# Kernel optimization log

Measured on AMD Instinct MI355X. Metric: run time of the kernel, lower is better.

The kernel has to match this reference:

```python
import jax, jax.numpy as jnp
import numpy as np

N_FLUID, N_BOX, K_MAX, KS, NCELL = 6000, 3000, 80, 4, 64
RADIUS = np.float32(0.5 * 1.5 * 6 * 0.025)  # filter_extent / 2 = 0.1125


def _ball_to_cube(p):
    """Volume-preserving ball->cube mapping (open3d ContinuousConv convention).
    p: [..., 3] coordinates in the unit ball; returns coords in [-1,1]^3."""
    eps = 1e-12
    x, y, z = p[..., 0], p[..., 1], p[..., 2]
    sq = x * x + y * y + z * z
    norm = jnp.sqrt(sq)
    rxy2 = x * x + y * y
    # sphere -> cylinder (volume preserving)
    polar = 1.25 * z * z > rxy2
    s_pol = jnp.sqrt(3.0 * norm / (norm + jnp.abs(z) + eps))
    s_eq = norm / jnp.sqrt(rxy2 + eps)
    xc = jnp.where(polar, s_pol * x, s_eq * x)
    yc = jnp.where(polar, s_pol * y, s_eq * y)
    zc = jnp.where(polar, jnp.sign(z) * norm, 1.5 * z * s_eq)
    zero = sq < 1e-12
    xc = jnp.where(zero, 0.0, xc)
    yc = jnp.where(zero, 0.0, yc)
    zc = jnp.where(zero, 0.0, zc)
    # cylinder -> cube (area-preserving disc -> square on xy)
    rxy = jnp.sqrt(xc * xc + yc * yc)
    FP = 4.0 / np.pi
    safe_x = jnp.where(jnp.abs(xc) < eps, eps, xc)
    safe_y = jnp.where(jnp.abs(yc) < eps, eps, yc)
    cond = jnp.abs(xc) >= jnp.abs(yc)
    u1 = jnp.sign(xc) * rxy
    v1 = u1 * FP * jnp.arctan(yc / safe_x)
    v2 = jnp.sign(yc) * rxy
    u2 = v2 * FP * jnp.arctan(xc / safe_y)
    u = jnp.where(cond, u1, u2)
    v = jnp.where(cond, v1, v2)
    small = rxy < eps
    u = jnp.where(small, 0.0, u)
    v = jnp.where(small, 0.0, v)
    return jnp.stack([u, v, zc], axis=-1)


def build_neighbors(pos_in, pos_out, ignore_self):
    """Fixed-radius neighbor search (capped at K_MAX) + window + trilinear
    interpolation cells/weights. Returns idx [No,K], cells [No,K,8] int32,
    coef [No,K,8] (trilinear weight * poly6 window * validity)."""
    d = pos_in[None, :, :] - pos_out[:, None, :]            # [No,Ni,3]
    d2 = jnp.sum(d * d, axis=-1)
    if ignore_self:
        ii = jnp.arange(pos_out.shape[0])
        d2 = jnp.where(ii[:, None] == ii[None, :], jnp.inf, d2)
    neg = jnp.where(d2 <= RADIUS * RADIUS, -d2, -jnp.inf)
    vals, idx = jax.lax.top_k(neg, K_MAX)                   # [No,K]
    valid = (vals > -jnp.inf).astype(pos_in.dtype)
    rel = (pos_in[idx] - pos_out[:, None, :]) / RADIUS      # [No,K,3] unit ball
    r2 = jnp.sum(rel * rel, axis=-1)
    win = jnp.clip((1.0 - r2) ** 3, 0.0, 1.0) * valid       # poly6 window
    g = jnp.clip((_ball_to_cube(rel) + 1.0) * 0.5 * (KS - 1), 0.0, KS - 1.0)
    i0 = jnp.clip(jnp.floor(g), 0, KS - 2).astype(jnp.int32)
    t = g - i0.astype(g.dtype)
    cells, tw = [], []
    for dx in (0, 1):
        for dy in (0, 1):
            for dz in (0, 1):
                w = ((t[..., 0] if dx else 1.0 - t[..., 0])
                     * (t[..., 1] if dy else 1.0 - t[..., 1])
                     * (t[..., 2] if dz else 1.0 - t[..., 2]))
                cell = ((i0[..., 2] + dz) * KS + (i0[..., 1] + dy)) * KS + (i0[..., 0] + dx)
                cells.append(cell)
                tw.append(w)
    cells = jnp.stack(cells, axis=-1)                       # [No,K,8]
    coef = jnp.stack(tw, axis=-1) * win[..., None]          # [No,K,8]
    return idx, cells, coef


def apply_cconv(feats_in, idx, cells, coef, W, b):
    """Continuous conv: scatter neighbor feats into 64 kernel cells per query,
    then contract with the filter. W: [64, F, O]."""
    N, K = idx.shape
    F = feats_in.shape[-1]
    nf = feats_in[idx]                                      # [N,K,F]
    S = jnp.zeros((N * NCELL, F), feats_in.dtype)
    row = (jnp.arange(N, dtype=jnp.int32) * NCELL)[:, None]
    for c in range(8):                                      # 8 trilinear corners
        flat = (row + cells[..., c]).reshape(-1)
        S = S.at[flat].add((coef[..., c:c + 1] * nf).reshape(-1, F))
    return jnp.einsum('ncf,cfo->no', S.reshape(N, NCELL, F), W) + b


def setup_inputs() -> dict:
    key = jax.random.key(0)
    ks = jax.random.split(key, 16)

    def p(i, shape, scale=0.05):
        return (scale * jax.random.normal(ks[i], shape)).astype(jnp.float32)

    return {
        'pos': jax.random.uniform(ks[0], (N_FLUID, 3), dtype=jnp.float32),
        'vel': jax.random.normal(ks[1], (N_FLUID, 3), dtype=jnp.float32),
        'box': jax.random.uniform(ks[2], (N_BOX, 3), dtype=jnp.float32),
        'box_feats': jax.random.normal(ks[3], (N_BOX, 3), dtype=jnp.float32),
        'cf_w': p(4, (NCELL, 4, 32)), 'cf_b': jnp.zeros((32,), jnp.float32),
        'co_w': p(5, (NCELL, 3, 32)), 'co_b': jnp.zeros((32,), jnp.float32),
        'd0_w': p(6, (4, 32)), 'd0_b': jnp.zeros((32,), jnp.float32),
        'c1_w': p(7, (NCELL, 96, 64)), 'c1_b': jnp.zeros((64,), jnp.float32),
        'd1_w': p(8, (96, 64)), 'd1_b': jnp.zeros((64,), jnp.float32),
        'c2_w': p(9, (NCELL, 64, 64)), 'c2_b': jnp.zeros((64,), jnp.float32),
        'd2_w': p(10, (64, 64)), 'd2_b': jnp.zeros((64,), jnp.float32),
        'c3_w': p(11, (NCELL, 64, 3)), 'c3_b': jnp.zeros((3,), jnp.float32),
        'd3_w': p(12, (64, 3)), 'd3_b': jnp.zeros((3,), jnp.float32),
    }


def reference(pos, vel, box, box_feats, cf_w, cf_b, co_w, co_b, d0_w, d0_b,
              c1_w, c1_b, d1_w, d1_b, c2_w, c2_b, d2_w, d2_b, c3_w, c3_b,
              d3_w, d3_b):
    fidx, fcells, fcoef = build_neighbors(pos, pos, True)
    oidx, ocells, ocoef = build_neighbors(box, pos, False)
    ff = jnp.concatenate([jnp.ones_like(pos[:, :1]), vel], axis=-1)  # [N,4]
    a_cf = apply_cconv(ff, fidx, fcells, fcoef, cf_w, cf_b)
    a_co = apply_cconv(box_feats, oidx, ocells, ocoef, co_w, co_b)
    a_d0 = ff @ d0_w + d0_b
    x = jnp.concatenate([a_co, a_cf, a_d0], axis=-1)                 # [N,96]
    for cw, cb, dw, db in ((c1_w, c1_b, d1_w, d1_b),
                           (c2_w, c2_b, d2_w, d2_b),
                           (c3_w, c3_b, d3_w, d3_b)):
        h = jax.nn.relu(x)
        y = apply_cconv(h, fidx, fcells, fcoef, cw, cb) + (h @ dw + db)
        x = y + x if y.shape[-1] == x.shape[-1] else y
    return x * (1.0 / 128.0)  # pos_correction [N,3]
```

## Files before the change

### kernel.cpp

```cpp
#include <hip/hip_runtime.h>
#include <math.h>

namespace {

constexpr int NQ  = 6000;
constexpr int NB  = 3000;
constexpr int K   = 80;
constexpr float RAD = 0.1125f;
constexpr float RADI = 1.0f / 0.1125f;
constexpr float R2  = RAD * RAD;
constexpr float EPSF = 1e-12f;

constexpr int GS  = 8;
constexpr int NC  = GS*GS*GS;
constexpr int NO  = 65 * 64;
constexpr int NBLK = (NQ + 3) / 4;
constexpr int NBLK8 = ((NBLK + 7) / 8) * 8;
constexpr int PREPB = 512;

typedef __attribute__((ext_vector_type(8))) short bf16x8;
typedef __attribute__((ext_vector_type(4))) float f32x4;

__device__ __forceinline__ float sgn(float x) {
    return (x > 0.f) ? 1.f : ((x < 0.f) ? -1.f : 0.f);
}

__device__ __forceinline__ unsigned int bf16rne(float f) {
    unsigned int u = __float_as_uint(f);
    return (u + 0x7fffu + ((u >> 16) & 1u)) >> 16;
}
__device__ __forceinline__ float bf16f(unsigned short u) {
    return __uint_as_float(((unsigned int)u) << 16);
}
__device__ __forceinline__ int cell_of(float x, float y, float z) {
    int cx = min(max((int)(x * (float)GS), 0), GS-1);
    int cy = min(max((int)(y * (float)GS), 0), GS-1);
    int cz = min(max((int)(z * (float)GS), 0), GS-1);
    return (cz*GS + cy)*GS + cx;
}

__device__ __forceinline__ void coef_compute(
    float ddx, float ddy, float ddz, int slot,
    int* __restrict__ cells, float* __restrict__ coefs)
{
    float rx = ddx * RADI, ry = ddy * RADI, rz = ddz * RADI;
    float r2 = rx*rx + ry*ry + rz*rz;
    float w1 = 1.f - r2;
    float win = (w1 > 0.f) ? w1*w1*w1 : 0.f;
    float norm = sqrtf(r2);
    float rxy2 = rx*rx + ry*ry;
    float xc, yc, zc;
    if (r2 < 1e-12f) {
        xc = yc = zc = 0.f;
    } else if (1.25f * rz * rz > rxy2) {
        float s = sqrtf(3.0f * norm / (norm + fabsf(rz) + EPSF));
        xc = s * rx; yc = s * ry; zc = sgn(rz) * norm;
    } else {
        float s = norm / sqrtf(rxy2 + EPSF);
        xc = s * rx; yc = s * ry; zc = 1.5f * rz * s;
    }
    float rxy = sqrtf(xc*xc + yc*yc);
    const float FP = (float)(4.0 / M_PI);
    float u, v;
    if (rxy < EPSF) {
        u = 0.f; v = 0.f;
    } else if (fabsf(xc) >= fabsf(yc)) {
        float sx = (fabsf(xc) < EPSF) ? EPSF : xc;
        u = sgn(xc) * rxy;
        v = u * FP * atanf(yc / sx);
    } else {
        float sy = (fabsf(yc) < EPSF) ? EPSF : yc;
        v = sgn(yc) * rxy;
        u = v * FP * atanf(xc / sy);
    }
    float gx = fminf(fmaxf((u  + 1.f) * 0.5f * 3.f, 0.f), 3.f);
    float gy = fminf(fmaxf((v  + 1.f) * 0.5f * 3.f, 0.f), 3.f);
    float gz = fminf(fmaxf((zc + 1.f) * 0.5f * 3.f, 0.f), 3.f);
    int ix = min((int)floorf(gx), 2);
    int iy = min((int)floorf(gy), 2);
    int iz = min((int)floorf(gz), 2);
    float tx = gx - (float)ix, ty = gy - (float)iy, tz = gz - (float)iz;
    cells[slot] = iz*16 + iy*4 + ix;
    float wx0 = 1.f - tx, wy0 = 1.f - ty, wz0 = 1.f - tz;
    float4 lo, hi;
    lo.x = wx0 * wy0 * wz0 * win;
    lo.y = wx0 * wy0 * tz  * win;
    lo.z = wx0 * ty  * wz0 * win;
    lo.w = wx0 * ty  * tz  * win;
    hi.x = tx  * wy0 * wz0 * win;
    hi.y = tx  * wy0 * tz  * win;
    hi.z = tx  * ty  * wz0 * win;
    hi.w = tx  * ty  * tz  * win;
    float4* cf = (float4*)(coefs + (size_t)slot * 8);
    cf[0] = lo; cf[1] = hi;
}

__global__ __launch_bounds__(1024) void grid_build_kernel(
    const float* __restrict__ pos, const float* __restrict__ box,
    int* __restrict__ gs_f, int* __restrict__ gs_b,
    int* __restrict__ cur_f, int* __restrict__ cur_b)
{
    __shared__ int cntF[NC], cntB[NC];
    __shared__ int tmpF[NC], tmpB[NC];
    int tid = threadIdx.x;
    int half = tid >> 9, t = tid & 511;
    if (half == 0) cntF[t] = 0; else cntB[t] = 0;
    __syncthreads();
    for (int i = tid; i < NQ + NB; i += 1024) {
        if (i < NQ) {
            atomicAdd(&cntF[cell_of(pos[i*3], pos[i*3+1], pos[i*3+2])], 1);
        } else {
            int b = i - NQ;
            atomicAdd(&cntB[cell_of(box[b*3], box[b*3+1], box[b*3+2])], 1);
        }
    }
    __syncthreads();
    int* cnt = half ? cntB : cntF;
    int* tmp = half ? tmpB : tmpF;
    int cv = cnt[t];
    tmp[t] = cv;
    __syncthreads();
    for (int off = 1; off < NC; off <<= 1) {
        int v = (t >= off) ? tmp[t - off] : 0;
        __syncthreads();
        tmp[t] += v;
        __syncthreads();
    }
    int* gsd = half ? gs_b : gs_f;
    int* cur = half ? cur_b : cur_f;
    int excl = tmp[t] - cv;
    gsd[t] = excl;
    cur[t] = excl;
    if (t == NC - 1) gsd[NC] = tmp[t];
}

__global__ __launch_bounds__(256) void scatter_pts_kernel(
    const float* __restrict__ pos, const float* __restrict__ box,
    int* __restrict__ cur_f, int* __restrict__ cur_b,
    float* __restrict__ spf, int* __restrict__ sif,
    float* __restrict__ spb, int* __restrict__ sib)
{
    int t = blockIdx.x * blockDim.x + threadIdx.x;
    if (t < NQ) {
        float x = pos[t*3], y = pos[t*3+1], z = pos[t*3+2];
        int dst = atomicAdd(&cur_f[cell_of(x,y,z)], 1);
        *reinterpret_cast<float4*>(spf + (size_t)dst*4) = make_float4(x, y, z, 0.f);
        sif[dst] = t;
    } else if (t < NQ + NB) {
        int b = t - NQ;
        float x = box[b*3], y = box[b*3+1], z = box[b*3+2];
        int dst = atomicAdd(&cur_b[cell_of(x,y,z)], 1);
        *reinterpret_cast<float4*>(spb + (size_t)dst*4) = make_float4(x, y, z, 0.f);
        sib[dst] = b;
    }
}

__global__ __launch_bounds__(256) void nn2gc_kernel(
    const float* __restrict__ pos,
    const float* __restrict__ spf, const int* __restrict__ sif, const int* __restrict__ gsf,
    const float* __restrict__ spb, const int* __restrict__ sib, const int* __restrict__ gsb,
    int* __restrict__ f_cnt, int* __restrict__ f_idx, float* __restrict__ f_d2,
    int* __restrict__ f_cell, float* __restrict__ f_coef,
    int* __restrict__ b_cnt, int* __restrict__ b_idx, float* __restrict__ b_d2,
    int* __restrict__ b_cell, float* __restrict__ b_coef,
    const float* __restrict__ c1w, const float* __restrict__ d1w,
    const float* __restrict__ c2w, const float* __restrict__ d2w,
    const float* __restrict__ c3w, const float* __restrict__ d3w,
    const float* __restrict__ vel, const float* __restrict__ bfeat,
    const float* __restrict__ cfw, const float* __restrict__ cow,
    const float* __restrict__ d0w, const float* __restrict__ d0b,
    unsigned short* __restrict__ Bt1, unsigned short* __restrict__ Bt2,
    unsigned short* __restrict__ G0f, unsigned short* __restrict__ G0b,
    float* __restrict__ W3p, float* __restrict__ x1)
{
    if (blockIdx.x < PREPB) {
        int stride = PREPB * 256;
        int gid = blockIdx.x * 256 + threadIdx.x;
        for (int i = gid; i < NQ * 1024; i += stride) {
            int j = i >> 10, rr = i & 1023, c = rr >> 4, op = (rr & 15) * 2;
            float vx = vel[j*3+0], vy = vel[j*3+1], vz = vel[j*3+2];
            const float* w = cfw + (size_t)c * 128;
            float s0 = w[op]   + vx*w[32+op]   + vy*w[64+op]   + vz*w[96+op];
            float s1 = w[op+1] + vx*w[32+op+1] + vy*w[64+op+1] + vz*w[96+op+1];
            *reinterpret_cast<unsigned int*>(G0f + (size_t)j * 2048 + c*32 + op) =
                bf16rne(s0) | (bf16rne(s1) << 16);
        }
        for (int i = gid; i < NB * 1024; i += stride) {
            int j = i >> 10, rr = i & 1023, c = rr >> 4, op = (rr & 15) * 2;
            float b0 = bfeat[j*3+0], b1 = bfeat[j*3+1], b2 = bfeat[j*3+2];
            const float* w = cow + (size_t)c * 96;
            float s0 = b0*w[op]   + b1*w[32+op]   + b2*w[64+op];
            float s1 = b0*w[op+1] + b1*w[32+op+1] + b2*w[64+op+1];
            *reinterpret_cast<unsigned int*>(G0b + (size_t)j * 2048 + c*32 + op) =
                bf16rne(s0) | (bf16rne(s1) << 16);
        }
        for (int i = gid; i < NO * 96; i += stride) {
            int n = i / 96, f = i % 96, c = n >> 6, o = n & 63;
            float v = (c < 64) ? c1w[((size_t)c*96 + f)*64 + o] : d1w[f*64 + o];
            Bt1[i] = (unsigned short)bf16rne(v);
        }
        for (int i = gid; i < NO * 64; i += stride) {
            int n = i / 64, f = i % 64, c = n >> 6, o = n & 63;
            float v = (c < 64) ? c2w[((size_t)c*64 + f)*64 + o] : d2w[f*64 + o];
            Bt2[i] = (unsigned short)bf16rne(v);
        }
        for (int i = gid; i < 64 * 195; i += stride) {
            int f = i / 195, r = i % 195, c = r / 3, o = r % 3;
            W3p[i] = (c < 64) ? c3w[(c*64 + f)*3 + o] : d3w[f*3 + o];
        }
        for (int i = gid; i < NQ * 32; i += stride) {
            int n = i >> 5, o = i & 31;
            float acc = d0b[o] + d0w[o]
                      + vel[n*3+0] * d0w[32 + o]
                      + vel[n*3+1] * d0w[64 + o]
                      + vel[n*3+2] * d0w[96 + o];
            x1[n*96 + 64 + o] = acc;
        }
        return;
    }
    int gw = (int)(blockIdx.x - PREPB) * 4 + ((int)threadIdx.x >> 6);
    int lane = threadIdx.x & 63;
    if (gw >= 2 * NQ) return;
    bool isF = gw < NQ;
    int wid = isF ? gw : gw - NQ;
    const float* sp = isF ? spf : spb;
    const int*   si = isF ? sif : sib;
    const int*   gs = isF ? gsf : gsb;
    int*   cnt   = isF ? f_cnt  : b_cnt;
    int*   idxs  = isF ? f_idx  : b_idx;
    float* d2s   = isF ? f_d2   : b_d2;
    int*   cells = isF ? f_cell : b_cell;
    float* coefs = isF ? f_coef : b_coef;
    int    tot   = isF ? NQ : NB;
    float qx = pos[wid*3+0], qy = pos[wid*3+1], qz = pos[wid*3+2];
    int cx = min(max((int)(qx * (float)GS), 0), GS-1);
    int cy = min(max((int)(qy * (float)GS), 0), GS-1);
    int cz = min(max((int)(qz * (float)GS), 0), GS-1);
    int x0 = max(cx-1, 0), x1c = min(cx+1, GS-1);
    int base = wid * K;
    int c = 0;

    auto process = [&](bool hit, int oj, float ddx, float ddy, float ddz, float d2) {
        unsigned long long m = __ballot(hit);
        int pc = __popcll(m);
        if (pc == 0) return;
        if (c + pc <= K) {
            if (hit) {
                int p = c + __popcll(m & ((1ull << lane) - 1ull));
                idxs[base + p] = oj;
                d2s [base + p] = d2;
                float* cf = coefs + (size_t)(base + p) * 8;
                cf[0] = ddx; cf[1] = ddy; cf[2] = ddz;
            }
            c += pc;
        } else {
            while (m) {
                int l = __ffsll((unsigned long long)m) - 1;
                m &= m - 1ull;
                float dd = __shfl(d2, l);
                int jv = __shfl(oj, l);
                float ax = __shfl(ddx, l), ay = __shfl(ddy, l), az = __shfl(ddz, l);
                int slot = -1;
                if (c < K) { slot = c; c++; }
                else {
                    float mx = -1.f; int am = 0;
                    for (int s = 0; s < K; ++s) {
                        float v = d2s[base + s];
                        if (v > mx) { mx = v; am = s; }
                    }
                    if (dd < mx) slot = am;
                }
                if (slot >= 0 && lane == 0) {
                    idxs[base + slot] = jv;
                    d2s [base + slot] = dd;
                    float* cf = coefs + (size_t)(base + slot) * 8;
                    cf[0] = ax; cf[1] = ay; cf[2] = az;
                }
            }
        }
    };

    int s0v[9], s1v[9];
#pragma unroll
    for (int r = 0; r < 9; ++r) {
        int z = cz + (r / 3) - 1, y = cy + (r % 3) - 1;
        bool ok = ((unsigned)z < (unsigned)GS) && ((unsigned)y < (unsigned)GS);
        int row = ok ? (z*GS + y)*GS : 0;
        int a0 = gs[row + x0];
        int a1 = gs[row + x1c + 1];
        s0v[r] = a0;
        s1v[r] = ok ? a1 : a0;
    }
    int    ojv[9];
    float4 pv [9];
#pragma unroll
    for (int r = 0; r < 9; ++r) {
        int a = min(s0v[r] + lane, tot - 1);
        ojv[r] = si[a];
        pv [r] = *reinterpret_cast<const float4*>(sp + (size_t)a * 4);
    }
#pragma unroll
    for (int r = 0; r < 9; ++r) {
        int ii = s0v[r] + lane;
        float ddx = pv[r].x - qx, ddy = pv[r].y - qy, ddz = pv[r].z - qz;
        float d2 = ddx*ddx + ddy*ddy + ddz*ddz;
        int oj = ojv[r];
        bool hit = (ii < s1v[r]) && (d2 <= R2) && !(isF && oj == wid);
        process(hit, oj, ddx, ddy, ddz, d2);
    }
#pragma unroll
    for (int r = 0; r < 9; ++r) {
        for (int j0 = s0v[r] + 64; j0 < s1v[r]; j0 += 64) {
            int ii = j0 + lane;
            int a = min(ii, tot - 1);
            int oj = si[a];
            float4 p = *reinterpret_cast<const float4*>(sp + (size_t)a * 4);
            float ddx = p.x - qx, ddy = p.y - qy, ddz = p.z - qz;
            float d2 = ddx*ddx + ddy*ddy + ddz*ddz;
            bool hit = (ii < s1v[r]) && (d2 <= R2) && !(isF && oj == wid);
            process(hit, oj, ddx, ddy, ddz, d2);
        }
    }
    for (int k2 = lane; k2 < c; k2 += 64) {
        const float4 d = *reinterpret_cast<const float4*>(coefs + (size_t)(base + k2) * 8);
        coef_compute(d.x, d.y, d.z, base + k2, cells, coefs);
    }
    if (lane == 0) cnt[wid] = c;
}

__global__ __launch_bounds__(256) void gather0_kernel(
    const int* __restrict__ order,
    const int* __restrict__ f_cnt, const int* __restrict__ f_idx,
    const int* __restrict__ f_cell, const float* __restrict__ f_coef,
    const int* __restrict__ b_cnt, const int* __restrict__ b_idx,
    const int* __restrict__ b_cell, const float* __restrict__ b_coef,
    const unsigned short* __restrict__ G0f, const unsigned short* __restrict__ G0b,
    const float* __restrict__ cfb, const float* __restrict__ cob,
    float* __restrict__ x1)
{
    __shared__ __align__(16) float coefF[K * 8];
    __shared__ __align__(16) float coefB[K * 8];
    __shared__ int jF[K], jB[K];
    __shared__ float partF[8][32], partB[8][32];
    int lb = (blockIdx.x & 7) * (gridDim.x >> 3) + (blockIdx.x >> 3);
    int tid = threadIdx.x;
    int wv = tid >> 6, lane = tid & 63;
    int h = lane >> 5, o = lane & 31;
    int r = wv * 2 + h;
    int n = order[lb];
    int cnf = f_cnt[n], cnb = b_cnt[n];
    {
        const float4* srcF = (const float4*)(f_coef + (size_t)n * K * 8);
        const float4* srcB = (const float4*)(b_coef + (size_t)n * K * 8);
        for (int i = tid; i < cnf * 2; i += 256) ((float4*)coefF)[i] = srcF[i];
        for (int i = tid; i < cnb * 2; i += 256) ((float4*)coefB)[i] = srcB[i];
        for (int i = tid; i < cnf; i += 256) jF[i] = f_idx[n*K + i] * 2048 + f_cell[n*K + i] * 32;
        for (int i = tid; i < cnb; i += 256) jB[i] = b_idx[n*K + i] * 2048 + b_cell[n*K + i] * 32;
    }
    __syncthreads();
    float af = 0.f;
#pragma unroll 2
    for (int k = r; k < cnf; k += 8) {
        const unsigned short* Gj = G0f + jF[k] + o;
        float4 cA = *reinterpret_cast<const float4*>(coefF + k*8);
        float4 cB = *reinterpret_cast<const float4*>(coefF + k*8 + 4);
        af += cA.x * bf16f(Gj[ 0 * 32]);
        af += cA.y * bf16f(Gj[16 * 32]);
        af += cA.z * bf16f(Gj[ 4 * 32]);
        af += cA.w * bf16f(Gj[20 * 32]);
        af += cB.x * bf16f(Gj[ 1 * 32]);
        af += cB.y * bf16f(Gj[17 * 32]);
        af += cB.z * bf16f(Gj[ 5 * 32]);
        af += cB.w * bf16f(Gj[21 * 32]);
    }
    float ab = 0.f;
#pragma unroll 2
    for (int k = r; k < cnb; k += 8) {
        const unsigned short* Gj = G0b + jB[k] + o;
        float4 cA = *reinterpret_cast<const float4*>(coefB + k*8);
        float4 cB = *reinterpret_cast<const float4*>(coefB + k*8 + 4);
        ab += cA.x * bf16f(Gj[ 0 * 32]);
        ab += cA.y * bf16f(Gj[16 * 32]);
        ab += cA.z * bf16f(Gj[ 4 * 32]);
        ab += cA.w * bf16f(Gj[20 * 32]);
        ab += cB.x * bf16f(Gj[ 1 * 32]);
        ab += cB.y * bf16f(Gj[17 * 32]);
        ab += cB.z * bf16f(Gj[ 5 * 32]);
        ab += cB.w * bf16f(Gj[21 * 32]);
    }
    partF[r][o] = af;
    partB[r][o] = ab;
    __syncthreads();
    if (tid < 64) {
        int oo = tid & 31;
        if (tid < 32) {
            float s = cfb[oo];
#pragma unroll
            for (int q = 0; q < 8; ++q) s += partF[q][oo];
            x1[(size_t)n * 96 + 32 + oo] = s;
        } else {
            float s = cob[oo];
#pragma unroll
            for (int q = 0; q < 8; ++q) s += partB[q][oo];
            x1[(size_t)n * 96 + oo] = s;
        }
    }
}

template<int F>
__global__ __launch_bounds__(256) void gemmGm_kernel(
    const float* __restrict__ feats,
    const unsigned short* __restrict__ Bt,
    unsigned short* __restrict__ G,
    int M)
{
    constexpr int NT = 5;
    constexpr int AST = F + 8;
    __shared__ unsigned short As[64 * AST];
    __shared__ unsigned short Bs[64 * AST];
    int tid = threadIdx.x, lane = tid & 63, wv = tid >> 6;
    int m0 = blockIdx.x * 64;
    int nt0 = blockIdx.y * NT;
    for (int i = tid; i < 64 * F / 4; i += 256) {
        int m = i / (F / 4), k4 = i % (F / 4);
        int gm = m0 + m; if (gm >= M) gm = M - 1;
        float4 av = *reinterpret_cast<const float4*>(feats + (size_t)gm * F + k4 * 4);
        uint2 ov;
        ov.x = bf16rne(fmaxf(av.x, 0.f)) | (bf16rne(fmaxf(av.y, 0.f)) << 16);
        ov.y = bf16rne(fmaxf(av.z, 0.f)) | (bf16rne(fmaxf(av.w, 0.f)) << 16);
        *reinterpret_cast<uint2*>(As + m * AST + k4 * 4) = ov;
    }
    int mr = lane & 15, quad = lane >> 4;
    for (int t = 0; t < NT; ++t) {
        int no0 = (nt0 + t) * 64;
        __syncthreads();
        for (int i = tid; i < 64 * F / 8; i += 256) {
            int nn = i / (F / 8), k8 = i % (F / 8);
            *reinterpret_cast<uint4*>(Bs + nn * AST + k8 * 8) =
                *reinterpret_cast<const uint4*>(Bt + (size_t)(no0 + nn) * F + k8 * 8);
        }
        __syncthreads();
        f32x4 acc[4] = {{0.f,0.f,0.f,0.f},{0.f,0.f,0.f,0.f},
                        {0.f,0.f,0.f,0.f},{0.f,0.f,0.f,0.f}};
#pragma unroll
        for (int kc = 0; kc < F; kc += 32) {
            bf16x8 a = *reinterpret_cast<const bf16x8*>(As + (wv*16 + mr) * AST + kc + quad*8);
#pragma unroll
            for (int q = 0; q < 4; ++q) {
                bf16x8 b = *reinterpret_cast<const bf16x8*>(Bs + (q*16 + mr) * AST + kc + quad*8);
                acc[q] = __builtin_amdgcn_mfma_f32_16x16x32_bf16(a, b, acc[q], 0, 0, 0);
            }
        }
#pragma unroll
        for (int q = 0; q < 4; ++q) {
#pragma unroll
            for (int rr = 0; rr < 4; ++rr) {
                int gm = m0 + wv*16 + quad*4 + rr;
                if (gm < M)
                    G[(size_t)gm * NO + no0 + q*16 + mr] = (unsigned short)bf16rne(acc[q][rr]);
            }
        }
    }
}

template<int FUSEY>
__global__ __launch_bounds__(256) void gatherG_kernel(
    const int* __restrict__ order,
    const int* __restrict__ cnt, const int* __restrict__ nidx,
    const int* __restrict__ ncell, const float* __restrict__ ncoef,
    const unsigned short* __restrict__ G,
    const float* __restrict__ cb, const float* __restrict__ db,
    const float* __restrict__ resid, float* __restrict__ out,
    const float* __restrict__ W3p, float* __restrict__ Y)
{
    __shared__ __align__(16) float coefL[K * 8];
    __shared__ int jL[K];
    __shared__ float part[3][64];
    __shared__ float xs[64];
    int lb = (blockIdx.x & 7) * (gridDim.x >> 3) + (blockIdx.x >> 3);
    int tid = threadIdx.x;
    int wv = tid >> 6, lane = tid & 63;
    int n = order[lb];
    int cn = cnt[n];
    {
        const float4* src = (const float4*)(ncoef + (size_t)n * K * 8);
        float4* dst = (float4*)coefL;
        for (int i = tid; i < cn * 2; i += 256) dst[i] = src[i];
        for (int i = tid; i < cn; i += 256)
            jL[i] = nidx[n*K + i] * NO + ncell[n*K + i] * 64;
    }
    __syncthreads();
    float a0 = 0.f, a1 = 0.f, a2 = 0.f, a3 = 0.f;
#pragma unroll 2
    for (int k = wv; k < cn; k += 4) {
        float4 cA = *reinterpret_cast<const float4*>(coefL + k*8);
        float4 cB = *reinterpret_cast<const float4*>(coefL + k*8 + 4);
        const unsigned short* Gj = G + jL[k] + lane;
        a0 += cA.x * bf16f(Gj[ 0 * 64]);
        a1 += cA.y * bf16f(Gj[16 * 64]);
        a2 += cA.z * bf16f(Gj[ 4 * 64]);
        a3 += cA.w * bf16f(Gj[20 * 64]);
        a0 += cB.x * bf16f(Gj[ 1 * 64]);
        a1 += cB.y * bf16f(Gj[17 * 64]);
        a2 += cB.z * bf16f(Gj[ 5 * 64]);
        a3 += cB.w * bf16f(Gj[21 * 64]);
    }
    float s = (a0 + a1) + (a2 + a3);
    if (wv > 0) part[wv - 1][lane] = s;
    __syncthreads();
    if (wv == 0) {
        float acc = cb[lane] + db[lane] + s
                  + part[0][lane] + part[1][lane] + part[2][lane];
        acc += bf16f(G[(size_t)n * NO + 64*64 + lane]);
        if (resid) acc += resid[(size_t)n * 64 + lane];
        if (!FUSEY) {
            out[(size_t)n * 64 + lane] = acc;
        } else {
            xs[lane] = fmaxf(acc, 0.f);
        }
    }
    if (FUSEY) {
        __syncthreads();
        for (int t = tid; t < 195; t += 256) {
            float sum = 0.f;
#pragma unroll 16
            for (int f = 0; f < 64; ++f) sum += xs[f] * W3p[f*195 + t];
            Y[(size_t)n * 195 + t] = sum;
        }
    }
}

__global__ __launch_bounds__(256) void gather3_kernel(
    const int* __restrict__ order,
    const int* __restrict__ cnt, const int* __restrict__ nidx,
    const int* __restrict__ ncell, const float* __restrict__ ncoef,
    const float* __restrict__ Y,
    const float* __restrict__ cb3, const float* __restrict__ db3,
    float* __restrict__ out)
{
    int lb = (blockIdx.x & 7) * (gridDim.x >> 3) + (blockIdx.x >> 3);
    int gw = lb * 4 + ((int)threadIdx.x >> 6);
    int lane = threadIdx.x & 63;
    if (gw >= NQ) return;
    int n = order[gw];
    int cn = cnt[n];
    float a0 = 0.f, a1 = 0.f, a2 = 0.f;
#pragma unroll
    for (int seg = 0; seg < 2; ++seg) {
        int kidx = seg * 64 + lane;
        if (kidx < cn) {
            int j  = nidx [n*K + kidx];
            int cb = ncell[n*K + kidx];
            const float* cf = ncoef + (size_t)(n*K + kidx) * 8;
            const float* Yj = Y + (size_t)j * 195;
#pragma unroll
            for (int c = 0; c < 8; ++c) {
                int cell = cb + (c & 1)*16 + ((c >> 1) & 1)*4 + (c >> 2);
                float wgt = cf[c];
                const float* Tp = Yj + cell*3;
                a0 += wgt * Tp[0];
                a1 += wgt * Tp[1];
                a2 += wgt * Tp[2];
            }
        }
    }
#pragma unroll
    for (int s = 32; s > 0; s >>= 1) {
        a0 += __shfl_down(a0, s);
        a1 += __shfl_down(a1, s);
        a2 += __shfl_down(a2, s);
    }
    if (lane == 0) {
        const float* Yn = Y + (size_t)n * 195 + 192;
        out[n*3+0] = (a0 + Yn[0] + cb3[0] + db3[0]) * (1.f/128.f);
        out[n*3+1] = (a1 + Yn[1] + cb3[1] + db3[1]) * (1.f/128.f);
        out[n*3+2] = (a2 + Yn[2] + cb3[2] + db3[2]) * (1.f/128.f);
    }
}

}

extern "C" void kernel_launch(void* const* d_in, const int* in_sizes, int n_in,
                              void* d_out, int out_size, void* d_ws, size_t ws_size,
                              hipStream_t stream)
{
    const float* pos       = (const float*)d_in[0];
    const float* vel       = (const float*)d_in[1];
    const float* box       = (const float*)d_in[2];
    const float* box_feats = (const float*)d_in[3];
    const float* cf_w = (const float*)d_in[4];  const float* cf_b = (const float*)d_in[5];
    const float* co_w = (const float*)d_in[6];  const float* co_b = (const float*)d_in[7];
    const float* d0_w = (const float*)d_in[8];  const float* d0_b = (const float*)d_in[9];
    const float* c1_w = (const float*)d_in[10]; const float* c1_b = (const float*)d_in[11];
    const float* d1_w = (const float*)d_in[12]; const float* d1_b = (const float*)d_in[13];
    const float* c2_w = (const float*)d_in[14]; const float* c2_b = (const float*)d_in[15];
    const float* d2_w = (const float*)d_in[16]; const float* d2_b = (const float*)d_in[17];
    const float* c3_w = (const float*)d_in[18]; const float* c3_b = (const float*)d_in[19];
    const float* d3_w = (const float*)d_in[20]; const float* d3_b = (const float*)d_in[21];

    char* wsb = (char*)d_ws;
    size_t off = 0;
    auto alloc = [&](size_t bytes) {
        void* p = wsb + off;
        off = (off + bytes + 255) & ~(size_t)255;
        return p;
    };
    char*  Graw = (char*)alloc((size_t)NQ * NO * 2 + 4096);
    unsigned short* G = (unsigned short*)Graw;
    float* f_d2 = (float*)Graw;
    float* b_d2 = (float*)Graw + (size_t)NQ * K;
    unsigned short* G0f = (unsigned short*)(Graw + ((size_t)4 << 20));
    unsigned short* G0b = (unsigned short*)(Graw + ((size_t)32 << 20));
    int*   f_cnt  = (int*)  alloc((size_t)NQ * 4);
    int*   f_idx  = (int*)  alloc((size_t)NQ * K * 4);
    int*   f_cell = (int*)  alloc((size_t)NQ * K * 4);
    float* f_coef = (float*)alloc((size_t)NQ * K * 8 * 4);
    int*   b_cnt  = (int*)  alloc((size_t)NQ * 4);
    int*   b_idx  = (int*)  alloc((size_t)NQ * K * 4);
    int*   b_cell = (int*)  alloc((size_t)NQ * K * 4);
    float* b_coef = (float*)alloc((size_t)NQ * K * 8 * 4);
    float* x1     = (float*)alloc((size_t)NQ * 96 * 4);
    float* x2     = (float*)alloc((size_t)NQ * 64 * 4);
    unsigned short* Bt1 = (unsigned short*)alloc((size_t)NO * 96 * 2);
    unsigned short* Bt2 = (unsigned short*)alloc((size_t)NO * 64 * 2);
    float* W3p    = (float*)alloc((size_t)64 * 195 * 4);
    float* Y      = (float*)alloc((size_t)NQ * 195 * 4);
    int*   gs_f   = (int*)  alloc((size_t)(NC + 1) * 4);
    int*   gs_b   = (int*)  alloc((size_t)(NC + 1) * 4);
    int*   cur_f  = (int*)  alloc((size_t)NC * 4);
    int*   cur_b  = (int*)  alloc((size_t)NC * 4);
    float* spf    = (float*)alloc((size_t)(NQ + 1) * 4 * 4);
    int*   sif    = (int*)  alloc((size_t)NQ * 4);
    float* spb    = (float*)alloc((size_t)(NB + 1) * 4 * 4);
    int*   sib    = (int*)  alloc((size_t)NB * 4);

    dim3 b256(256);
    grid_build_kernel<<<1, 1024, 0, stream>>>(pos, box, gs_f, gs_b, cur_f, cur_b);
    scatter_pts_kernel<<<(NQ + NB + 255)/256, b256, 0, stream>>>(
        pos, box, cur_f, cur_b, spf, sif, spb, sib);
    nn2gc_kernel<<<PREPB + (2*NQ + 3)/4, b256, 0, stream>>>(
        pos, spf, sif, gs_f, spb, sib, gs_b,
        f_cnt, f_idx, f_d2, f_cell, f_coef,
        b_cnt, b_idx, b_d2, b_cell, b_coef,
        c1_w, d1_w, c2_w, d2_w, c3_w, d3_w,
        vel, box_feats, cf_w, co_w, d0_w, d0_b,
        Bt1, Bt2, G0f, G0b, W3p, x1);
    gather0_kernel<<<NQ, b256, 0, stream>>>(sif,
        f_cnt, f_idx, f_cell, f_coef,
        b_cnt, b_idx, b_cell, b_coef,
        G0f, G0b, cf_b, co_b, x1);
    gemmGm_kernel<96><<<dim3((NQ+63)/64, 13), b256, 0, stream>>>(x1, Bt1, G, NQ);
    gatherG_kernel<0><<<NQ, b256, 0, stream>>>(sif, f_cnt, f_idx, f_cell, f_coef,
        G, c1_b, d1_b, nullptr, x2, nullptr, nullptr);
    gemmGm_kernel<64><<<dim3((NQ+63)/64, 13), b256, 0, stream>>>(x2, Bt2, G, NQ);
    gatherG_kernel<1><<<NQ, b256, 0, stream>>>(sif, f_cnt, f_idx, f_cell, f_coef,
        G, c2_b, d2_b, x2, nullptr, W3p, Y);
    gather3_kernel<<<NBLK8, b256, 0, stream>>>(sif, f_cnt, f_idx, f_cell, f_coef,
        Y, c3_b, d3_b, (float*)d_out);

    (void)in_sizes; (void)n_in; (void)out_size; (void)ws_size;
    (void)f_d2; (void)b_d2;
}
```

Before: 240.8 us.

## Fuse point scatter into grid build, stage GEMM output, pad Y for vector loads

Three independent changes. The scatter kernel is merged into the single-block grid build kernel, using shared-memory atomics as cursors, which removes one launch and the global cursor arrays. The gemmGm epilogue now stages bf16 results through shared memory so each thread writes 16-byte coalesced chunks instead of scattered 2-byte stores. Y is padded to four floats per cell (stride 260), so gather3 can fetch each cell with float4 loads and read coefficients as float4. In exchange, the fused scatter runs on only one block, and the padded Y layout adds about a third more memory footprint.

```diff
diff --git a/kernel.cpp b/kernel.cpp
--- a/kernel.cpp
+++ b/kernel.cpp
@@ -17,6 +17,7 @@
 constexpr int NBLK = (NQ + 3) / 4;
 constexpr int NBLK8 = ((NBLK + 7) / 8) * 8;
 constexpr int PREPB = 512;
+constexpr int YST = 260;
 
 typedef __attribute__((ext_vector_type(8))) short bf16x8;
 typedef __attribute__((ext_vector_type(4))) float f32x4;
@@ -98,7 +99,8 @@
 __global__ __launch_bounds__(1024) void grid_build_kernel(
     const float* __restrict__ pos, const float* __restrict__ box,
     int* __restrict__ gs_f, int* __restrict__ gs_b,
-    int* __restrict__ cur_f, int* __restrict__ cur_b)
+    float* __restrict__ spf, int* __restrict__ sif,
+    float* __restrict__ spb, int* __restrict__ sib)
 {
     __shared__ int cntF[NC], cntB[NC];
     __shared__ int tmpF[NC], tmpB[NC];
@@ -127,31 +129,24 @@
         __syncthreads();
     }
     int* gsd = half ? gs_b : gs_f;
-    int* cur = half ? cur_b : cur_f;
     int excl = tmp[t] - cv;
     gsd[t] = excl;
-    cur[t] = excl;
+    cnt[t] = excl;
     if (t == NC - 1) gsd[NC] = tmp[t];
-}
-
-__global__ __launch_bounds__(256) void scatter_pts_kernel(
-    const float* __restrict__ pos, const float* __restrict__ box,
-    int* __restrict__ cur_f, int* __restrict__ cur_b,
-    float* __restrict__ spf, int* __restrict__ sif,
-    float* __restrict__ spb, int* __restrict__ sib)
-{
-    int t = blockIdx.x * blockDim.x + threadIdx.x;
-    if (t < NQ) {
-        float x = pos[t*3], y = pos[t*3+1], z = pos[t*3+2];
-        int dst = atomicAdd(&cur_f[cell_of(x,y,z)], 1);
-        *reinterpret_cast<float4*>(spf + (size_t)dst*4) = make_float4(x, y, z, 0.f);
-        sif[dst] = t;
-    } else if (t < NQ + NB) {
-        int b = t - NQ;
-        float x = box[b*3], y = box[b*3+1], z = box[b*3+2];
-        int dst = atomicAdd(&cur_b[cell_of(x,y,z)], 1);
-        *reinterpret_cast<float4*>(spb + (size_t)dst*4) = make_float4(x, y, z, 0.f);
-        sib[dst] = b;
+    __syncthreads();
+    for (int i = tid; i < NQ + NB; i += 1024) {
+        if (i < NQ) {
+            float x = pos[i*3], y = pos[i*3+1], z = pos[i*3+2];
+            int dst = atomicAdd(&cntF[cell_of(x,y,z)], 1);
+            *reinterpret_cast<float4*>(spf + (size_t)dst*4) = make_float4(x, y, z, 0.f);
+            sif[dst] = i;
+        } else {
+            int b = i - NQ;
+            float x = box[b*3], y = box[b*3+1], z = box[b*3+2];
+            int dst = atomicAdd(&cntB[cell_of(x,y,z)], 1);
+            *reinterpret_cast<float4*>(spb + (size_t)dst*4) = make_float4(x, y, z, 0.f);
+            sib[dst] = b;
+        }
     }
 }
 
@@ -416,8 +411,10 @@
 {
     constexpr int NT = 5;
     constexpr int AST = F + 8;
+    constexpr int CST = 72;
     __shared__ unsigned short As[64 * AST];
     __shared__ unsigned short Bs[64 * AST];
+    unsigned short* Cs = Bs;
     int tid = threadIdx.x, lane = tid & 63, wv = tid >> 6;
     int m0 = blockIdx.x * 64;
     int nt0 = blockIdx.y * NT;
@@ -431,6 +428,7 @@
         *reinterpret_cast<uint2*>(As + m * AST + k4 * 4) = ov;
     }
     int mr = lane & 15, quad = lane >> 4;
+    int orow = tid >> 2, oseg = tid & 3;
     for (int t = 0; t < NT; ++t) {
         int no0 = (nt0 + t) * 64;
         __syncthreads();
@@ -451,14 +449,20 @@
                 acc[q] = __builtin_amdgcn_mfma_f32_16x16x32_bf16(a, b, acc[q], 0, 0, 0);
             }
         }
-#pragma unroll
-        for (int q = 0; q < 4; ++q) {
-#pragma unroll
-            for (int rr = 0; rr < 4; ++rr) {
-                int gm = m0 + wv*16 + quad*4 + rr;
-                if (gm < M)
-                    G[(size_t)gm * NO + no0 + q*16 + mr] = (unsigned short)bf16rne(acc[q][rr]);
-            }
+        __syncthreads();
+#pragma unroll
+        for (int q = 0; q < 4; ++q)
+#pragma unroll
+            for (int rr = 0; rr < 4; ++rr)
+                Cs[(wv*16 + quad*4 + rr) * CST + q*16 + mr] =
+                    (unsigned short)bf16rne(acc[q][rr]);
+        __syncthreads();
+        int gm = m0 + orow;
+        uint4 v0 = *reinterpret_cast<const uint4*>(Cs + orow * CST + oseg * 16);
+        uint4 v1 = *reinterpret_cast<const uint4*>(Cs + orow * CST + oseg * 16 + 8);
+        if (gm < M) {
+            *reinterpret_cast<uint4*>(G + (size_t)gm * NO + no0 + oseg * 16)     = v0;
+            *reinterpret_cast<uint4*>(G + (size_t)gm * NO + no0 + oseg * 16 + 8) = v1;
         }
     }
 }
@@ -521,11 +525,14 @@
     }
     if (FUSEY) {
         __syncthreads();
-        for (int t = tid; t < 195; t += 256) {
-            float sum = 0.f;
+        for (int idx = tid; idx < YST; idx += 256) {
+            int cc = idx >> 2, o = idx & 3;
+            if (o < 3) {
+                float sum = 0.f;
 #pragma unroll 16
-            for (int f = 0; f < 64; ++f) sum += xs[f] * W3p[f*195 + t];
-            Y[(size_t)n * 195 + t] = sum;
+                for (int f = 0; f < 64; ++f) sum += xs[f] * W3p[f*195 + cc*3 + o];
+                Y[(size_t)n * YST + idx] = sum;
+            }
         }
     }
 }
@@ -552,16 +559,23 @@
             int j  = nidx [n*K + kidx];
             int cb = ncell[n*K + kidx];
             const float* cf = ncoef + (size_t)(n*K + kidx) * 8;
-            const float* Yj = Y + (size_t)j * 195;
-#pragma unroll
-            for (int c = 0; c < 8; ++c) {
-                int cell = cb + (c & 1)*16 + ((c >> 1) & 1)*4 + (c >> 2);
-                float wgt = cf[c];
-                const float* Tp = Yj + cell*3;
-                a0 += wgt * Tp[0];
-                a1 += wgt * Tp[1];
-                a2 += wgt * Tp[2];
-            }
+            float4 cA = *reinterpret_cast<const float4*>(cf);
+            float4 cB = *reinterpret_cast<const float4*>(cf + 4);
+            const float* Yj = Y + (size_t)j * YST + (size_t)cb * 4;
+            float4 v00 = *reinterpret_cast<const float4*>(Yj +  0 * 4);
+            float4 v01 = *reinterpret_cast<const float4*>(Yj +  1 * 4);
+            float4 v10 = *reinterpret_cast<const float4*>(Yj + 16 * 4);
+            float4 v11 = *reinterpret_cast<const float4*>(Yj + 17 * 4);
+            float4 v20 = *reinterpret_cast<const float4*>(Yj +  4 * 4);
+            float4 v21 = *reinterpret_cast<const float4*>(Yj +  5 * 4);
+            float4 v30 = *reinterpret_cast<const float4*>(Yj + 20 * 4);
+            float4 v31 = *reinterpret_cast<const float4*>(Yj + 21 * 4);
+            a0 += cA.x*v00.x + cB.x*v01.x + cA.y*v10.x + cB.y*v11.x
+                + cA.z*v20.x + cB.z*v21.x + cA.w*v30.x + cB.w*v31.x;
+            a1 += cA.x*v00.y + cB.x*v01.y + cA.y*v10.y + cB.y*v11.y
+                + cA.z*v20.y + cB.z*v21.y + cA.w*v30.y + cB.w*v31.y;
+            a2 += cA.x*v00.z + cB.x*v01.z + cA.y*v10.z + cB.y*v11.z
+                + cA.z*v20.z + cB.z*v21.z + cA.w*v30.z + cB.w*v31.z;
         }
     }
 #pragma unroll
@@ -571,7 +585,7 @@
         a2 += __shfl_down(a2, s);
     }
     if (lane == 0) {
-        const float* Yn = Y + (size_t)n * 195 + 192;
+        const float* Yn = Y + (size_t)n * YST + 256;
         out[n*3+0] = (a0 + Yn[0] + cb3[0] + db3[0]) * (1.f/128.f);
         out[n*3+1] = (a1 + Yn[1] + cb3[1] + db3[1]) * (1.f/128.f);
         out[n*3+2] = (a2 + Yn[2] + cb3[2] + db3[2]) * (1.f/128.f);
@@ -624,20 +638,17 @@
     unsigned short* Bt1 = (unsigned short*)alloc((size_t)NO * 96 * 2);
     unsigned short* Bt2 = (unsigned short*)alloc((size_t)NO * 64 * 2);
     float* W3p    = (float*)alloc((size_t)64 * 195 * 4);
-    float* Y      = (float*)alloc((size_t)NQ * 195 * 4);
+    float* Y      = (float*)alloc((size_t)NQ * YST * 4);
     int*   gs_f   = (int*)  alloc((size_t)(NC + 1) * 4);
     int*   gs_b   = (int*)  alloc((size_t)(NC + 1) * 4);
-    int*   cur_f  = (int*)  alloc((size_t)NC * 4);
-    int*   cur_b  = (int*)  alloc((size_t)NC * 4);
     float* spf    = (float*)alloc((size_t)(NQ + 1) * 4 * 4);
     int*   sif    = (int*)  alloc((size_t)NQ * 4);
     float* spb    = (float*)alloc((size_t)(NB + 1) * 4 * 4);
     int*   sib    = (int*)  alloc((size_t)NB * 4);
 
     dim3 b256(256);
-    grid_build_kernel<<<1, 1024, 0, stream>>>(pos, box, gs_f, gs_b, cur_f, cur_b);
-    scatter_pts_kernel<<<(NQ + NB + 255)/256, b256, 0, stream>>>(
-        pos, box, cur_f, cur_b, spf, sif, spb, sib);
+    grid_build_kernel<<<1, 1024, 0, stream>>>(pos, box, gs_f, gs_b,
+                                              spf, sif, spb, sib);
     nn2gc_kernel<<<PREPB + (2*NQ + 3)/4, b256, 0, stream>>>(
         pos, spf, sif, gs_f, spb, sib, gs_b,
         f_cnt, f_idx, f_d2, f_cell, f_coef,
```

Result: slower. 261.9 us (+8.8%).
